# Kernel optimization log

Hardware: AMD Instinct MI355X
Metric: run time of the kernel (lower is better)

## Reference

```python
import jax, jax.numpy as jnp
import numpy as np

CHUNK = 64  # chunk_size
EPS = 1e-6


def setup_inputs() -> dict:
    key = jax.random.key(0)
    ks = jax.random.split(key, 7)
    b, L, H, dh, ds = 2, 4096, 16, 64, 64
    X = jax.random.normal(ks[0], (b, L, H, dh), dtype=jnp.float32)
    # negative log-decay in (-1, 0) for numerical stability (Mamba2 convention)
    A = -jax.random.uniform(ks[1], (b, L, H), dtype=jnp.float32)
    B = jax.random.normal(ks[2], (b, L, H, ds), dtype=jnp.float32)
    C = jax.random.normal(ks[3], (b, L, H, ds), dtype=jnp.float32)
    log2_alpha_base = jnp.full((H,), -0.15, dtype=jnp.float32) + 0.02 * jax.random.normal(ks[4], (H,), dtype=jnp.float32)
    log2_beta = 0.02 * jax.random.normal(ks[5], (H,), dtype=jnp.float32)
    surprise_ema = jnp.ones((H,), dtype=jnp.float32)
    return {"X": X, "A": A, "B": B, "C": C,
            "log2_alpha_base": log2_alpha_base, "log2_beta": log2_beta,
            "surprise_ema": surprise_ema}


def reference(X, A, B, C, log2_alpha_base, log2_beta, surprise_ema):
    b, L, H, dh = X.shape
    ds = B.shape[-1]
    n = L // CHUNK  # L is a multiple of CHUNK (no padding needed)

    # [b, h, n, c, ...] layout
    Xt = X.reshape(b, n, CHUNK, H, dh).transpose(0, 3, 1, 2, 4)   # b h n c dh
    At = A.reshape(b, n, CHUNK, H).transpose(0, 3, 1, 2)          # b h n c
    Bt = B.reshape(b, n, CHUNK, H, ds).transpose(0, 3, 1, 2, 4)   # b h n c ds
    Ct = C.reshape(b, n, CHUNK, H, ds).transpose(0, 3, 1, 2, 4)   # b h n c ds

    # per-chunk surprise from outer-product state delta
    BX = jnp.einsum('bhncs,bhncd->bhnsd', Bt, Xt)                 # b h n ds dh
    chunk_surprise = (BX ** 2).mean(axis=(-1, -2))                # b h n

    # surprise gate (eval mode: EMA buffer not updated)
    normalized = chunk_surprise / (surprise_ema[None, :, None] + EPS)
    log2c = jnp.clip(log2_alpha_base, -3.32, -0.015)
    alpha_base = 1.0 - jnp.exp2(log2c)                            # [H]
    beta = jnp.exp2(jnp.clip(log2_beta, -2.0, 2.0))               # [H]
    boost = jax.nn.relu(jnp.tanh(beta[None, :, None] * normalized))
    alpha = jnp.clip(alpha_base[None, :, None]
                     + (1.0 - alpha_base[None, :, None]) * boost, 0.01, 0.999)

    # surprise-modulated decay
    A_mod = At * (1.0 - alpha)[..., None]                         # b h n c
    A_cs = jnp.cumsum(A_mod, axis=-1)                             # b h n c

    # intra-chunk attention-like term with causal decay matrix
    diff = A_cs[..., :, None] - A_cs[..., None, :]                # b h n c c
    causal = jnp.tril(jnp.ones((CHUNK, CHUNK), dtype=bool))
    Lmat = jnp.where(causal, jnp.exp(diff), 0.0)
    CB = jnp.einsum('bhnid,bhnjd->bhnij', Ct, Bt)
    Y_intra = jnp.einsum('bhnij,bhnjd->bhnid', Lmat * CB, Xt)

    # inter-chunk state carry (sequential over chunks)
    decay_chunk = jnp.exp(A_mod.sum(axis=-1))                     # b h n
    decay_to_end = jnp.exp(A_cs[..., -1:] - A_cs)                 # b h n c
    h_final = jnp.einsum('bhnc,bhncs,bhncd->bhnsd', decay_to_end, Bt, Xt)

    def step(carry, inp):
        dc, hf = inp                                              # dc: b h ; hf: b h ds dh
        return dc[..., None, None] * carry + hf, carry

    dc_n = jnp.moveaxis(decay_chunk, 2, 0)                        # n b h
    hf_n = jnp.moveaxis(h_final, 2, 0)                            # n b h ds dh
    init = jnp.zeros((b, H, ds, dh), X.dtype)
    _, h_inter_n = jax.lax.scan(step, init, (dc_n, hf_n))
    h_inter = jnp.moveaxis(h_inter_n, 0, 2)                       # b h n ds dh

    decay_from_start = jnp.exp(A_cs)
    Y_inter = jnp.einsum('bhnis,bhnsp,bhni->bhnip', Ct, h_inter, decay_from_start)

    Y = (Y_intra + Y_inter).transpose(0, 2, 3, 1, 4).reshape(b, L, H, dh)
    return Y
```

## Files before the change

### kernel.cpp

```cpp
#include <hip/hip_runtime.h>
#include <hip/hip_bf16.h>
#include <math.h>

#define LSEQ 4096
#define NH   16
#define DH   64
#define CH   64
#define NCH  64

typedef __attribute__((ext_vector_type(8))) short bf16x8;
typedef __attribute__((ext_vector_type(4))) short s16x4;
typedef __attribute__((ext_vector_type(4))) float f32x4;

#define MFMA16(a, b, c) __builtin_amdgcn_mfma_f32_16x16x32_bf16((a), (b), (c), 0, 0, 0)

__device__ __forceinline__ int swz(int row, int col) {
    return (row << 6) + (col ^ ((row & 7) << 3));
}

__device__ __forceinline__ float4 ld4(const float* p) {
    return *reinterpret_cast<const float4*>(p);
}
__device__ __forceinline__ short f2b(float x) {
    __hip_bfloat16 h = __float2bfloat16(x);
    return *reinterpret_cast<short*>(&h);
}
__device__ __forceinline__ float b2f(short s) {
    union { unsigned u; float f; } v;
    v.u = ((unsigned)(unsigned short)s) << 16;
    return v.f;
}
__device__ __forceinline__ s16x4 pack4(float a, float b, float c, float d) {
    s16x4 r; r.x = f2b(a); r.y = f2b(b); r.z = f2b(c); r.w = f2b(d); return r;
}
__device__ __forceinline__ uint2 sx2(uint2 v, int m) {
    uint2 r;
    r.x = (unsigned)__shfl_xor((int)v.x, m, 64);
    r.y = (unsigned)__shfl_xor((int)v.y, m, 64);
    return r;
}
__device__ __forceinline__ short ext4(uint2 u, int g) {
    unsigned word = (g & 2) ? u.y : u.x;
    return (short)((g & 1) ? (word >> 16) : (word & 0xffffu));
}

__global__ __launch_bounds__(256) void ssd_k1(
    const float* __restrict__ X, const float* __restrict__ A,
    const float* __restrict__ B, const float* __restrict__ C,
    const float* __restrict__ l2ab, const float* __restrict__ l2b,
    const float* __restrict__ ema,
    unsigned short* __restrict__ yw, unsigned short* __restrict__ hf,
    float* __restrict__ dcb, float* __restrict__ dfs)
{
    __shared__ __align__(16) short R1[CH * 64];
    __shared__ __align__(16) short R2[CH * 64];
    __shared__ __align__(16) short R3[CH * 64];
    __shared__ __align__(16) short R4[CH * 64];
    __shared__ __align__(16) short R5[CH * 64];

    const int tid  = threadIdx.x;
    const int blk  = blockIdx.x;
    const int nidx = blk & (NCH - 1);
    const int h    = (blk >> 6) & (NH - 1);
    const int bb   = blk >> 10;
    const size_t base = ((size_t)(bb * LSEQ + nidx * CH) * NH + h) * DH;

    const int lane = tid & 63;
    const int w    = tid >> 6;
    const int rb   = 16 * w;
    const int fr   = lane & 15;
    const int gq   = lane >> 4;
    const int g4   = 4 * gq;
    const int ko   = 8 * gq;
    const int rot  = (fr >> 1) & 3;

    const int sc = tid >> 4, sd0 = (tid & 15) * 4;

    #pragma unroll
    for (int m = 0; m < 4; ++m) {
        int c = sc + 16 * m;
        size_t g = base + (size_t)c * 1024 + sd0;
        float4 xv = ld4(&X[g]);
        float4 bv = ld4(&B[g]);
        float4 cv = ld4(&C[g]);
        *reinterpret_cast<s16x4*>(&R1[swz(c, sd0)]) = pack4(xv.x, xv.y, xv.z, xv.w);
        *reinterpret_cast<s16x4*>(&R2[swz(c, sd0)]) = pack4(bv.x, bv.y, bv.z, bv.w);
        *reinterpret_cast<s16x4*>(&R3[swz(c, sd0)]) = pack4(cv.x, cv.y, cv.z, cv.w);
    }
    float aval = A[(size_t)(bb * LSEQ + nidx * CH + lane) * NH + h];
    __syncthreads();

    float cum = aval;
    #pragma unroll
    for (int off = 1; off < 64; off <<= 1) {
        float t = __shfl_up(cum, off, 64);
        if (lane >= off) cum += t;
    }
    float cum_tot = __shfl(cum, 63, 64);

    const f32x4 zf = {0.f, 0.f, 0.f, 0.f};

    float ss = 0.f;
    #pragma unroll
    for (int m = 0; m < 4; ++m) {
        bf16x8 aXm0 = *reinterpret_cast<const bf16x8*>(&R1[swz(16 * m + fr, 0  + ko)]);
        bf16x8 aXm1 = *reinterpret_cast<const bf16x8*>(&R1[swz(16 * m + fr, 32 + ko)]);
        bf16x8 aBm0 = *reinterpret_cast<const bf16x8*>(&R2[swz(16 * m + fr, 0  + ko)]);
        bf16x8 aBm1 = *reinterpret_cast<const bf16x8*>(&R2[swz(16 * m + fr, 32 + ko)]);
        #pragma unroll
        for (int n = 0; n < 4; ++n) {
            bf16x8 bX0 = *reinterpret_cast<const bf16x8*>(&R1[swz(16 * n + fr, 0  + ko)]);
            bf16x8 bX1 = *reinterpret_cast<const bf16x8*>(&R1[swz(16 * n + fr, 32 + ko)]);
            bf16x8 bB0 = *reinterpret_cast<const bf16x8*>(&R2[swz(16 * n + fr, 0  + ko)]);
            bf16x8 bB1 = *reinterpret_cast<const bf16x8*>(&R2[swz(16 * n + fr, 32 + ko)]);
            f32x4 gx = MFMA16(aXm1, bX1, MFMA16(aXm0, bX0, zf));
            f32x4 gb = MFMA16(aBm1, bB1, MFMA16(aBm0, bB0, zf));
            #pragma unroll
            for (int r = 0; r < 4; ++r) ss = fmaf(gx[r], gb[r], ss);
        }
    }
    #pragma unroll
    for (int off = 32; off > 0; off >>= 1) ss += __shfl_xor(ss, off, 64);

    bf16x8 aC0 = *reinterpret_cast<const bf16x8*>(&R3[swz(rb + fr, 0  + ko)]);
    bf16x8 aC1 = *reinterpret_cast<const bf16x8*>(&R3[swz(rb + fr, 32 + ko)]);
    f32x4 aCB[4];
    #pragma unroll
    for (int n = 0; n < 4; ++n) {
        bf16x8 bB0 = *reinterpret_cast<const bf16x8*>(&R2[swz(16 * n + fr, 0  + ko)]);
        bf16x8 bB1 = *reinterpret_cast<const bf16x8*>(&R2[swz(16 * n + fr, 32 + ko)]);
        aCB[n] = MFMA16(aC1, bB1, MFMA16(aC0, bB0, zf));
    }

    s16x4 outB[4];
    const int d0 = 4 * fr;
    #pragma unroll
    for (int m = 0; m < 4; ++m) {
        int c0 = 16 * w + 4 * ((m + rot) & 3);
        uint2 mx = *reinterpret_cast<const uint2*>(&R1[swz(c0 + gq, d0)]);
        uint2 mb = *reinterpret_cast<const uint2*>(&R2[swz(c0 + gq, d0)]);
        uint2 px_ = sx2(mx, 16), pb_ = sx2(mb, 16);
        uint2 xe = (gq & 1) ? px_ : mx, xo = (gq & 1) ? mx : px_;
        uint2 be = (gq & 1) ? pb_ : mb, bo = (gq & 1) ? mb : pb_;
        uint2 xpe = sx2(xe, 32), xpo = sx2(xo, 32);
        uint2 bpe = sx2(be, 32), bpo = sx2(bo, 32);
        uint2 xr0 = (gq & 2) ? xpe : xe, xr1 = (gq & 2) ? xpo : xo;
        uint2 xr2 = (gq & 2) ? xe : xpe, xr3 = (gq & 2) ? xo : xpo;
        uint2 br0 = (gq & 2) ? bpe : be, br1 = (gq & 2) ? bpo : bo;
        uint2 br2 = (gq & 2) ? be : bpe, br3 = (gq & 2) ? bo : bpo;
        s16x4 ox; ox.x = ext4(xr0, gq); ox.y = ext4(xr1, gq);
                  ox.z = ext4(xr2, gq); ox.w = ext4(xr3, gq);
        *reinterpret_cast<s16x4*>(&R4[swz(d0 + gq, c0)]) = ox;
        s16x4 ob; ob.x = ext4(br0, gq); ob.y = ext4(br1, gq);
                  ob.z = ext4(br2, gq); ob.w = ext4(br3, gq);
        outB[m] = ob;
    }

    float surprise = ss * (1.f / 4096.f);
    float l2c   = fminf(fmaxf(l2ab[h], -3.32f), -0.015f);
    float ab_   = 1.f - exp2f(l2c);
    float bt    = exp2f(fminf(fmaxf(l2b[h], -2.f), 2.f));
    float nrm   = surprise / (ema[h] + 1e-6f);
    float boost = fmaxf(tanhf(bt * nrm), 0.f);
    float alpha = fminf(fmaxf(ab_ + (1.f - ab_) * boost, 0.01f), 0.999f);
    float scale = 1.f - alpha;
    float v    = cum * scale;
    float tot  = cum_tot * scale;
    float epv  = __expf(v);
    float env  = __expf(-v);
    float dtev = __expf(tot - v);
    if (w == 0) {
        dfs[(size_t)blk * CH + lane] = epv;
        if (lane == 63) dcb[blk] = __expf(tot);
    }

    {
        float epi[4], enj[4];
        #pragma unroll
        for (int r = 0; r < 4; ++r) epi[r] = __shfl(epv, rb + g4 + r, 64);
        #pragma unroll
        for (int n = 0; n < 4; ++n) enj[n] = __shfl(env, 16 * n + fr, 64);
        #pragma unroll
        for (int n = 0; n < 4; ++n)
            #pragma unroll
            for (int r = 0; r < 4; ++r) {
                int i = rb + g4 + r, j = 16 * n + fr;
                float val = (j <= i) ? epi[r] * enj[n] * aCB[n][r] : 0.f;
                R3[swz(i, j)] = f2b(val);
            }
    }

    #pragma unroll
    for (int m = 0; m < 4; ++m) {
        int c0 = 16 * w + 4 * ((m + rot) & 3);
        float dt0 = __shfl(dtev, c0 + 0, 64), dt1 = __shfl(dtev, c0 + 1, 64);
        float dt2 = __shfl(dtev, c0 + 2, 64), dt3 = __shfl(dtev, c0 + 3, 64);
        s16x4 ob;
        ob.x = f2b(b2f(outB[m].x) * dt0);
        ob.y = f2b(b2f(outB[m].y) * dt1);
        ob.z = f2b(b2f(outB[m].z) * dt2);
        ob.w = f2b(b2f(outB[m].w) * dt3);
        *reinterpret_cast<s16x4*>(&R5[swz(d0 + gq, c0)]) = ob;
    }
    __syncthreads();

    f32x4 acc2[4] = {zf, zf, zf, zf};
    f32x4 acc3[4] = {zf, zf, zf, zf};
    #pragma unroll
    for (int k0 = 0; k0 < 64; k0 += 32) {
        bf16x8 aX = *reinterpret_cast<const bf16x8*>(&R4[swz(rb + fr, k0 + ko)]);
        bf16x8 aB = *reinterpret_cast<const bf16x8*>(&R5[swz(rb + fr, k0 + ko)]);
        #pragma unroll
        for (int n = 0; n < 4; ++n) {
            bf16x8 bT = *reinterpret_cast<const bf16x8*>(&R3[swz(16 * n + fr, k0 + ko)]);
            bf16x8 bX = *reinterpret_cast<const bf16x8*>(&R4[swz(16 * n + fr, k0 + ko)]);
            acc2[n] = MFMA16(aX, bT, acc2[n]);
            acc3[n] = MFMA16(aB, bX, acc3[n]);
        }
    }
    #pragma unroll
    for (int n = 0; n < 4; ++n) {
        int colI = 16 * n + fr;
        s16x4 y4 = pack4(acc2[n][0], acc2[n][1], acc2[n][2], acc2[n][3]);
        s16x4 h4 = pack4(acc3[n][0], acc3[n][1], acc3[n][2], acc3[n][3]);
        *reinterpret_cast<s16x4*>(&yw[(size_t)blk * 4096 + colI * 64 + rb + g4]) = y4;
        *reinterpret_cast<s16x4*>(&hf[(size_t)blk * 4096 + colI * 64 + rb + g4]) = h4;
    }
}

__global__ __launch_bounds__(256) void ssd_k2(
    unsigned int* __restrict__ hfU, const float* __restrict__ dcb)
{
    __shared__ float sdc[NCH];
    const int tid = threadIdx.x;
    const int bh  = blockIdx.x >> 3;
    const int sub = blockIdx.x & 7;
    if (tid < NCH) sdc[tid] = dcb[bh * NCH + tid];
    __syncthreads();
    const size_t base = (size_t)bh * NCH * 2048 + sub * 256 + tid;

    float c0 = 0.f, c1 = 0.f;
    unsigned int cur[8];
    #pragma unroll
    for (int kk = 0; kk < 8; ++kk) cur[kk] = hfU[base + (size_t)kk * 2048];
    #pragma unroll
    for (int kb = 0; kb < 8; ++kb) {
        unsigned int nxt[8];
        if (kb < 7) {
            #pragma unroll
            for (int kk = 0; kk < 8; ++kk)
                nxt[kk] = hfU[base + (size_t)(8 * kb + 8 + kk) * 2048];
        }
        #pragma unroll
        for (int kk = 0; kk < 8; ++kk) {
            int k = 8 * kb + kk;
            unsigned int u = cur[kk];
            union { unsigned int q; float f; } lo, hi;
            lo.q = u << 16;
            hi.q = u & 0xffff0000u;
            unsigned int packed = (unsigned int)(unsigned short)f2b(c0)
                                | ((unsigned int)(unsigned short)f2b(c1) << 16);
            hfU[base + (size_t)k * 2048] = packed;
            float d = sdc[k];
            c0 = fmaf(d, c0, lo.f);
            c1 = fmaf(d, c1, hi.f);
        }
        if (kb < 7) {
            #pragma unroll
            for (int kk = 0; kk < 8; ++kk) cur[kk] = nxt[kk];
        }
    }
}

__global__ __launch_bounds__(256) void ssd_k3(
    const float* __restrict__ C, const unsigned short* __restrict__ hI,
    const unsigned short* __restrict__ yw, const float* __restrict__ dfs,
    float* __restrict__ Y)
{
    __shared__ __align__(16) short sHt[CH * 64];
    __shared__ __align__(16) short sC2[CH * 64];
    __shared__ float sF[CH];

    const int tid  = threadIdx.x;
    const int blk  = blockIdx.x;
    const int nidx = blk & (NCH - 1);
    const int h    = (blk >> 6) & (NH - 1);
    const int bb   = blk >> 10;
    const size_t base = ((size_t)(bb * LSEQ + nidx * CH) * NH + h) * DH;

    #pragma unroll
    for (int m = 0; m < 2; ++m) {
        int idx = tid + 256 * m;
        int row = idx >> 3, c8 = (idx & 7) * 8;
        bf16x8 v = *reinterpret_cast<const bf16x8*>(&hI[(size_t)blk * 4096 + row * 64 + c8]);
        *reinterpret_cast<bf16x8*>(&sHt[swz(row, c8)]) = v;
    }
    #pragma unroll
    for (int m = 0; m < 4; ++m) {
        int p = tid + 256 * m;
        int row = p >> 4, d0 = (p & 15) * 4;
        float4 cv = ld4(&C[base + (size_t)row * 1024 + d0]);
        *reinterpret_cast<s16x4*>(&sC2[swz(row, d0)]) = pack4(cv.x, cv.y, cv.z, cv.w);
    }
    if (tid < CH) sF[tid] = dfs[(size_t)blk * CH + tid];
    __syncthreads();

    const int lane = tid & 63;
    const int w    = tid >> 6;
    const int rb   = 16 * w;
    const int fr   = lane & 15;
    const int g4   = 4 * (lane >> 4);
    const int ko   = 8 * (lane >> 4);
    const f32x4 zf = {0.f, 0.f, 0.f, 0.f};

    f32x4 acc[4] = {zf, zf, zf, zf};
    #pragma unroll
    for (int k0 = 0; k0 < 64; k0 += 32) {
        bf16x8 a = *reinterpret_cast<const bf16x8*>(&sHt[swz(rb + fr, k0 + ko)]);
        #pragma unroll
        for (int n = 0; n < 4; ++n) {
            bf16x8 b = *reinterpret_cast<const bf16x8*>(&sC2[swz(16 * n + fr, k0 + ko)]);
            acc[n] = MFMA16(a, b, acc[n]);
        }
    }
    #pragma unroll
    for (int n = 0; n < 4; ++n) {
        int i  = 16 * n + fr;
        int p0 = rb + g4;
        float f = sF[i];
        s16x4 y4 = *reinterpret_cast<const s16x4*>(&yw[(size_t)blk * 4096 + i * 64 + p0]);
        float4 o;
        o.x = fmaf(f, acc[n][0], b2f(y4.x));
        o.y = fmaf(f, acc[n][1], b2f(y4.y));
        o.z = fmaf(f, acc[n][2], b2f(y4.z));
        o.w = fmaf(f, acc[n][3], b2f(y4.w));
        *reinterpret_cast<float4*>(&Y[base + (size_t)i * 1024 + p0]) = o;
    }
}

extern "C" void kernel_launch(void* const* d_in, const int* in_sizes, int n_in,
                              void* d_out, int out_size, void* d_ws, size_t ws_size,
                              hipStream_t stream)
{
    const float* X    = (const float*)d_in[0];
    const float* A    = (const float*)d_in[1];
    const float* B    = (const float*)d_in[2];
    const float* C    = (const float*)d_in[3];
    const float* l2ab = (const float*)d_in[4];
    const float* l2b  = (const float*)d_in[5];
    const float* ema  = (const float*)d_in[6];
    float* Y = (float*)d_out;

    unsigned short* hf = (unsigned short*)d_ws;
    unsigned short* yw = hf + (size_t)8388608;
    float* dcb = (float*)(yw + (size_t)8388608);
    float* dfs = dcb + 2048;

    const int nblk = 2 * NH * NCH;
    ssd_k1<<<nblk, 256, 0, stream>>>(X, A, B, C, l2ab, l2b, ema, yw, hf, dcb, dfs);
    ssd_k2<<<256, 256, 0, stream>>>((unsigned int*)hf, dcb);
    ssd_k3<<<nblk, 256, 0, stream>>>(C, hf, yw, dfs, Y);
}
```

Baseline: 57.76 us.

## Split chunk kernel into separate gate and main kernels to cut LDS

Splits the first kernel in two. One computes the surprise gate and writes the per-position decay exponentials to workspace. The other reloads X, B and C and runs the intra-chunk and state MFMA work with four LDS buffers instead of five, reading the decay factors from global memory. This lowers shared memory per block and may allow higher occupancy, but X and B are now read twice, there is an extra kernel launch, and more decay arrays pass through global memory.

New measurement: 72.43 us. 25.4% more time.

```diff
diff --git a/kernel.cpp b/kernel.cpp
--- a/kernel.cpp
+++ b/kernel.cpp
@@ -44,19 +44,16 @@
     return (short)((g & 1) ? (word >> 16) : (word & 0xffffu));
 }
 
-__global__ __launch_bounds__(256) void ssd_k1(
+__global__ __launch_bounds__(256) void ssd_gate(
     const float* __restrict__ X, const float* __restrict__ A,
-    const float* __restrict__ B, const float* __restrict__ C,
+    const float* __restrict__ B,
     const float* __restrict__ l2ab, const float* __restrict__ l2b,
     const float* __restrict__ ema,
-    unsigned short* __restrict__ yw, unsigned short* __restrict__ hf,
-    float* __restrict__ dcb, float* __restrict__ dfs)
+    float* __restrict__ epvT, float* __restrict__ envT,
+    float* __restrict__ dteT, float* __restrict__ dcb)
 {
     __shared__ __align__(16) short R1[CH * 64];
     __shared__ __align__(16) short R2[CH * 64];
-    __shared__ __align__(16) short R3[CH * 64];
-    __shared__ __align__(16) short R4[CH * 64];
-    __shared__ __align__(16) short R5[CH * 64];
 
     const int tid  = threadIdx.x;
     const int blk  = blockIdx.x;
@@ -67,13 +64,8 @@
 
     const int lane = tid & 63;
     const int w    = tid >> 6;
-    const int rb   = 16 * w;
     const int fr   = lane & 15;
-    const int gq   = lane >> 4;
-    const int g4   = 4 * gq;
-    const int ko   = 8 * gq;
-    const int rot  = (fr >> 1) & 3;
-
+    const int ko   = 8 * (lane >> 4);
     const int sc = tid >> 4, sd0 = (tid & 15) * 4;
 
     #pragma unroll
@@ -82,10 +74,8 @@
         size_t g = base + (size_t)c * 1024 + sd0;
         float4 xv = ld4(&X[g]);
         float4 bv = ld4(&B[g]);
-        float4 cv = ld4(&C[g]);
         *reinterpret_cast<s16x4*>(&R1[swz(c, sd0)]) = pack4(xv.x, xv.y, xv.z, xv.w);
         *reinterpret_cast<s16x4*>(&R2[swz(c, sd0)]) = pack4(bv.x, bv.y, bv.z, bv.w);
-        *reinterpret_cast<s16x4*>(&R3[swz(c, sd0)]) = pack4(cv.x, cv.y, cv.z, cv.w);
     }
     float aval = A[(size_t)(bb * LSEQ + nidx * CH + lane) * NH + h];
     __syncthreads();
@@ -99,7 +89,6 @@
     float cum_tot = __shfl(cum, 63, 64);
 
     const f32x4 zf = {0.f, 0.f, 0.f, 0.f};
-
     float ss = 0.f;
     #pragma unroll
     for (int m = 0; m < 4; ++m) {
@@ -122,23 +111,86 @@
     #pragma unroll
     for (int off = 32; off > 0; off >>= 1) ss += __shfl_xor(ss, off, 64);
 
-    bf16x8 aC0 = *reinterpret_cast<const bf16x8*>(&R3[swz(rb + fr, 0  + ko)]);
-    bf16x8 aC1 = *reinterpret_cast<const bf16x8*>(&R3[swz(rb + fr, 32 + ko)]);
-    f32x4 aCB[4];
-    #pragma unroll
-    for (int n = 0; n < 4; ++n) {
-        bf16x8 bB0 = *reinterpret_cast<const bf16x8*>(&R2[swz(16 * n + fr, 0  + ko)]);
-        bf16x8 bB1 = *reinterpret_cast<const bf16x8*>(&R2[swz(16 * n + fr, 32 + ko)]);
-        aCB[n] = MFMA16(aC1, bB1, MFMA16(aC0, bB0, zf));
-    }
-
-    s16x4 outB[4];
+    float surprise = ss * (1.f / 4096.f);
+    float l2c   = fminf(fmaxf(l2ab[h], -3.32f), -0.015f);
+    float ab_   = 1.f - exp2f(l2c);
+    float bt    = exp2f(fminf(fmaxf(l2b[h], -2.f), 2.f));
+    float nrm   = surprise / (ema[h] + 1e-6f);
+    float boost = fmaxf(tanhf(bt * nrm), 0.f);
+    float alpha = fminf(fmaxf(ab_ + (1.f - ab_) * boost, 0.01f), 0.999f);
+    float scale = 1.f - alpha;
+    float v   = cum * scale;
+    float tot = cum_tot * scale;
+    if (w == 0) {
+        size_t o = (size_t)blk * CH + lane;
+        epvT[o] = __expf(v);
+        envT[o] = __expf(-v);
+        dteT[o] = __expf(tot - v);
+        if (lane == 63) dcb[blk] = __expf(tot);
+    }
+}
+
+__global__ __launch_bounds__(256) void ssd_main(
+    const float* __restrict__ X, const float* __restrict__ B,
+    const float* __restrict__ C,
+    const float* __restrict__ epvT, const float* __restrict__ envT,
+    const float* __restrict__ dteT,
+    unsigned short* __restrict__ yw, unsigned short* __restrict__ hf)
+{
+    __shared__ __align__(16) short R1[CH * 64];
+    __shared__ __align__(16) short R2[CH * 64];
+    __shared__ __align__(16) short R3[CH * 64];
+    __shared__ __align__(16) short R4[CH * 64];
+
+    const int tid  = threadIdx.x;
+    const int blk  = blockIdx.x;
+    const int nidx = blk & (NCH - 1);
+    const int h    = (blk >> 6) & (NH - 1);
+    const int bb   = blk >> 10;
+    const size_t base = ((size_t)(bb * LSEQ + nidx * CH) * NH + h) * DH;
+
+    const int lane = tid & 63;
+    const int w    = tid >> 6;
+    const int rb   = 16 * w;
+    const int fr   = lane & 15;
+    const int gq   = lane >> 4;
+    const int g4   = 4 * gq;
+    const int ko   = 8 * gq;
+    const int rot  = (fr >> 1) & 3;
+    const int sc = tid >> 4, sd0 = (tid & 15) * 4;
     const int d0 = 4 * fr;
+
+    size_t to = (size_t)blk * CH + lane;
+    float epvv = epvT[to];
+    float envv = envT[to];
+    float dtev = dteT[to];
+
     #pragma unroll
     for (int m = 0; m < 4; ++m) {
-        int c0 = 16 * w + 4 * ((m + rot) & 3);
-        uint2 mx = *reinterpret_cast<const uint2*>(&R1[swz(c0 + gq, d0)]);
-        uint2 mb = *reinterpret_cast<const uint2*>(&R2[swz(c0 + gq, d0)]);
+        int c = sc + 16 * m;
+        float4 cv = ld4(&C[base + (size_t)c * 1024 + sd0]);
+        *reinterpret_cast<s16x4*>(&R4[swz(c, sd0)]) = pack4(cv.x, cv.y, cv.z, cv.w);
+    }
+
+    uint2 qx[4], qb[4];
+    #pragma unroll
+    for (int mq = 0; mq < 4; ++mq) {
+        int row = 16 * w + 4 * mq + gq;
+        size_t g = base + (size_t)row * 1024 + d0;
+        float4 xv = ld4(&X[g]);
+        float4 bv = ld4(&B[g]);
+        s16x4 xp = pack4(xv.x, xv.y, xv.z, xv.w);
+        s16x4 bp = pack4(bv.x, bv.y, bv.z, bv.w);
+        qx[mq] = *reinterpret_cast<uint2*>(&xp);
+        qb[mq] = *reinterpret_cast<uint2*>(&bp);
+        *reinterpret_cast<s16x4*>(&R3[swz(row, d0)]) = bp;
+    }
+
+    s16x4 outX[4], outB[4];
+    #pragma unroll
+    for (int mq = 0; mq < 4; ++mq) {
+        int c0 = 16 * w + 4 * mq;
+        uint2 mx = qx[mq], mb = qb[mq];
         uint2 px_ = sx2(mx, 16), pb_ = sx2(mb, 16);
         uint2 xe = (gq & 1) ? px_ : mx, xo = (gq & 1) ? mx : px_;
         uint2 be = (gq & 1) ? pb_ : mb, bo = (gq & 1) ? mb : pb_;
@@ -150,81 +202,86 @@
         uint2 br2 = (gq & 2) ? be : bpe, br3 = (gq & 2) ? bo : bpo;
         s16x4 ox; ox.x = ext4(xr0, gq); ox.y = ext4(xr1, gq);
                   ox.z = ext4(xr2, gq); ox.w = ext4(xr3, gq);
-        *reinterpret_cast<s16x4*>(&R4[swz(d0 + gq, c0)]) = ox;
-        s16x4 ob; ob.x = ext4(br0, gq); ob.y = ext4(br1, gq);
-                  ob.z = ext4(br2, gq); ob.w = ext4(br3, gq);
-        outB[m] = ob;
-    }
-
-    float surprise = ss * (1.f / 4096.f);
-    float l2c   = fminf(fmaxf(l2ab[h], -3.32f), -0.015f);
-    float ab_   = 1.f - exp2f(l2c);
-    float bt    = exp2f(fminf(fmaxf(l2b[h], -2.f), 2.f));
-    float nrm   = surprise / (ema[h] + 1e-6f);
-    float boost = fmaxf(tanhf(bt * nrm), 0.f);
-    float alpha = fminf(fmaxf(ab_ + (1.f - ab_) * boost, 0.01f), 0.999f);
-    float scale = 1.f - alpha;
-    float v    = cum * scale;
-    float tot  = cum_tot * scale;
-    float epv  = __expf(v);
-    float env  = __expf(-v);
-    float dtev = __expf(tot - v);
-    if (w == 0) {
-        dfs[(size_t)blk * CH + lane] = epv;
-        if (lane == 63) dcb[blk] = __expf(tot);
+        outX[mq] = ox;
+        float dt0 = __shfl(dtev, c0 + 0, 64), dt1 = __shfl(dtev, c0 + 1, 64);
+        float dt2 = __shfl(dtev, c0 + 2, 64), dt3 = __shfl(dtev, c0 + 3, 64);
+        s16x4 ob;
+        ob.x = f2b(b2f(ext4(br0, gq)) * dt0);
+        ob.y = f2b(b2f(ext4(br1, gq)) * dt1);
+        ob.z = f2b(b2f(ext4(br2, gq)) * dt2);
+        ob.w = f2b(b2f(ext4(br3, gq)) * dt3);
+        outB[mq] = ob;
+    }
+    #pragma unroll
+    for (int mm = 0; mm < 4; ++mm) {
+        int mq = (mm + rot) & 3;
+        int c0 = 16 * w + 4 * mq;
+        *reinterpret_cast<s16x4*>(&R1[swz(d0 + gq, c0)]) = outX[mq];
+        *reinterpret_cast<s16x4*>(&R2[swz(d0 + gq, c0)]) = outB[mq];
+    }
+    __syncthreads();
+
+    const f32x4 zf = {0.f, 0.f, 0.f, 0.f};
+
+    f32x4 acc3[4] = {zf, zf, zf, zf};
+    #pragma unroll
+    for (int k0 = 0; k0 < 64; k0 += 32) {
+        bf16x8 aB = *reinterpret_cast<const bf16x8*>(&R2[swz(rb + fr, k0 + ko)]);
+        #pragma unroll
+        for (int n = 0; n < 4; ++n) {
+            bf16x8 bX = *reinterpret_cast<const bf16x8*>(&R1[swz(16 * n + fr, k0 + ko)]);
+            acc3[n] = MFMA16(aB, bX, acc3[n]);
+        }
+    }
+    #pragma unroll
+    for (int n = 0; n < 4; ++n) {
+        int colI = 16 * n + fr;
+        s16x4 h4 = pack4(acc3[n][0], acc3[n][1], acc3[n][2], acc3[n][3]);
+        *reinterpret_cast<s16x4*>(&hf[(size_t)blk * 4096 + colI * 64 + rb + g4]) = h4;
+    }
+
+    bf16x8 aC0 = *reinterpret_cast<const bf16x8*>(&R4[swz(rb + fr, 0  + ko)]);
+    bf16x8 aC1 = *reinterpret_cast<const bf16x8*>(&R4[swz(rb + fr, 32 + ko)]);
+    f32x4 aCB[4];
+    #pragma unroll
+    for (int n = 0; n < 4; ++n) {
+        bf16x8 bB0 = *reinterpret_cast<const bf16x8*>(&R3[swz(16 * n + fr, 0  + ko)]);
+        bf16x8 bB1 = *reinterpret_cast<const bf16x8*>(&R3[swz(16 * n + fr, 32 + ko)]);
+        aCB[n] = MFMA16(aC1, bB1, MFMA16(aC0, bB0, zf));
     }
 
     {
         float epi[4], enj[4];
         #pragma unroll
-        for (int r = 0; r < 4; ++r) epi[r] = __shfl(epv, rb + g4 + r, 64);
-        #pragma unroll
-        for (int n = 0; n < 4; ++n) enj[n] = __shfl(env, 16 * n + fr, 64);
+        for (int r = 0; r < 4; ++r) epi[r] = __shfl(epvv, rb + g4 + r, 64);
+        #pragma unroll
+        for (int n = 0; n < 4; ++n) enj[n] = __shfl(envv, 16 * n + fr, 64);
         #pragma unroll
         for (int n = 0; n < 4; ++n)
             #pragma unroll
             for (int r = 0; r < 4; ++r) {
                 int i = rb + g4 + r, j = 16 * n + fr;
                 float val = (j <= i) ? epi[r] * enj[n] * aCB[n][r] : 0.f;
-                R3[swz(i, j)] = f2b(val);
+                R4[swz(i, j)] = f2b(val);
             }
     }
-
-    #pragma unroll
-    for (int m = 0; m < 4; ++m) {
-        int c0 = 16 * w + 4 * ((m + rot) & 3);
-        float dt0 = __shfl(dtev, c0 + 0, 64), dt1 = __shfl(dtev, c0 + 1, 64);
-        float dt2 = __shfl(dtev, c0 + 2, 64), dt3 = __shfl(dtev, c0 + 3, 64);
-        s16x4 ob;
-        ob.x = f2b(b2f(outB[m].x) * dt0);
-        ob.y = f2b(b2f(outB[m].y) * dt1);
-        ob.z = f2b(b2f(outB[m].z) * dt2);
-        ob.w = f2b(b2f(outB[m].w) * dt3);
-        *reinterpret_cast<s16x4*>(&R5[swz(d0 + gq, c0)]) = ob;
-    }
     __syncthreads();
 
     f32x4 acc2[4] = {zf, zf, zf, zf};
-    f32x4 acc3[4] = {zf, zf, zf, zf};
     #pragma unroll
     for (int k0 = 0; k0 < 64; k0 += 32) {
-        bf16x8 aX = *reinterpret_cast<const bf16x8*>(&R4[swz(rb + fr, k0 + ko)]);
-        bf16x8 aB = *reinterpret_cast<const bf16x8*>(&R5[swz(rb + fr, k0 + ko)]);
+        bf16x8 aX = *reinterpret_cast<const bf16x8*>(&R1[swz(rb + fr, k0 + ko)]);
         #pragma unroll
         for (int n = 0; n < 4; ++n) {
-            bf16x8 bT = *reinterpret_cast<const bf16x8*>(&R3[swz(16 * n + fr, k0 + ko)]);
-            bf16x8 bX = *reinterpret_cast<const bf16x8*>(&R4[swz(16 * n + fr, k0 + ko)]);
+            bf16x8 bT = *reinterpret_cast<const bf16x8*>(&R4[swz(16 * n + fr, k0 + ko)]);
             acc2[n] = MFMA16(aX, bT, acc2[n]);
-            acc3[n] = MFMA16(aB, bX, acc3[n]);
         }
     }
     #pragma unroll
     for (int n = 0; n < 4; ++n) {
         int colI = 16 * n + fr;
         s16x4 y4 = pack4(acc2[n][0], acc2[n][1], acc2[n][2], acc2[n][3]);
-        s16x4 h4 = pack4(acc3[n][0], acc3[n][1], acc3[n][2], acc3[n][3]);
         *reinterpret_cast<s16x4*>(&yw[(size_t)blk * 4096 + colI * 64 + rb + g4]) = y4;
-        *reinterpret_cast<s16x4*>(&hf[(size_t)blk * 4096 + colI * 64 + rb + g4]) = h4;
     }
 }
 
@@ -353,11 +410,14 @@
 
     unsigned short* hf = (unsigned short*)d_ws;
     unsigned short* yw = hf + (size_t)8388608;
-    float* dcb = (float*)(yw + (size_t)8388608);
-    float* dfs = dcb + 2048;
+    float* epvT = (float*)(yw + (size_t)8388608);
+    float* envT = epvT + 131072;
+    float* dteT = envT + 131072;
+    float* dcb  = dteT + 131072;
 
     const int nblk = 2 * NH * NCH;
-    ssd_k1<<<nblk, 256, 0, stream>>>(X, A, B, C, l2ab, l2b, ema, yw, hf, dcb, dfs);
+    ssd_gate<<<nblk, 256, 0, stream>>>(X, A, B, l2ab, l2b, ema, epvT, envT, dteT, dcb);
+    ssd_main<<<nblk, 256, 0, stream>>>(X, B, C, epvT, envT, dteT, yw, hf);
     ssd_k2<<<256, 256, 0, stream>>>((unsigned int*)hf, dcb);
-    ssd_k3<<<nblk, 256, 0, stream>>>(C, hf, yw, dfs, Y);
-}
+    ssd_k3<<<nblk, 256, 0, stream>>>(C, hf, yw, epvT, Y);
+}
```
